# Performance work log

Measured on AMD Instinct MI355X. Metric: run time of the kernel, lower is better.

Reference implementation:

```python
import jax, jax.numpy as jnp
import numpy as np

HEADS = 8
DIM_HEAD = 64
LA = 0.33
LD = 0.33
LG = 0.33


def setup_inputs() -> dict:
    key = jax.random.key(0)
    ks = jax.random.split(key, 6)
    B, N, D = 4, 1024, 512
    inner = HEADS * DIM_HEAD
    x = jax.random.normal(ks[0], (B, N, D), jnp.float32)
    mask = jax.random.uniform(ks[1], (B, N)) < 0.9
    # sparse 0/1 molecular adjacency
    adjacency_mat = (jax.random.uniform(ks[2], (B, N, N)) < 0.05).astype(jnp.float32)
    # positive pairwise distances
    distance_mat = jax.random.uniform(ks[3], (B, N, N), jnp.float32) * 5.0
    W_qkv = jax.random.normal(ks[4], (D, inner * 3), jnp.float32) * 0.02
    W_out = jax.random.normal(ks[5], (inner, D), jnp.float32) * 0.02
    b_out = jnp.zeros((D,), jnp.float32)
    return {"x": x, "mask": mask, "adjacency_mat": adjacency_mat,
            "distance_mat": distance_mat, "W_qkv": W_qkv, "W_out": W_out, "b_out": b_out}


def reference(x, mask, adjacency_mat, distance_mat, W_qkv, W_out, b_out):
    B, N, _ = x.shape
    scale = DIM_HEAD ** -0.5
    # 'b n (h qkv d)' split: reshape to (B, N, H, 3, Dh) then move heads forward
    qkv = (x @ W_qkv).reshape(B, N, HEADS, 3, DIM_HEAD)
    q, k, v = (jnp.transpose(qkv[..., i, :], (0, 2, 1, 3)) for i in range(3))
    dots = jnp.einsum('bhid,bhjd->bhij', q, k) * scale  # [B,H,N,N]
    big = jnp.finfo(dots.dtype).max
    m2 = mask[:, None, :, None] & mask[:, None, None, :]  # [B,1,N,N]
    dots = jnp.where(m2, dots, -big)
    attn = jax.nn.softmax(dots, axis=-1) * LA
    # adjacency masked to 0; distance masked to +max so exp(-t) -> 0
    adj = jnp.where(m2, adjacency_mat[:, None], 0.0)
    dist = jnp.where(m2, distance_mat[:, None], big)
    attn = attn + LG * adj + LD * jnp.exp(-dist)
    out = jnp.einsum('bhij,bhjd->bhid', attn, v)
    out = jnp.transpose(out, (0, 2, 1, 3)).reshape(B, N, HEADS * DIM_HEAD)
    return out @ W_out + b_out
```

## Files before the change

### kernel.cpp

```cpp
#include <hip/hip_runtime.h>
#include <hip/hip_bf16.h>

typedef __attribute__((ext_vector_type(8))) __bf16 bf16x8;
typedef __attribute__((ext_vector_type(8))) unsigned short ushort8;
typedef __attribute__((ext_vector_type(4))) float f32x4;

#define DEVFN static __device__ __forceinline__

constexpr int B_ = 4, N_ = 1024, H_ = 8, DH_ = 64, INNER_ = 512, QC_ = 1536;
constexpr float LA_ = 0.33f, LD_ = 0.33f, LG_ = 0.33f;
constexpr float SCALE2_ = 0.125f * 1.44269504088896f;
constexpr long OCP_STRIDE_ = (long)4096 * 512;
constexpr long LP_STRIDE_  = (long)4 * 8 * 1024;

DEVFN unsigned short f2b(float f){
  unsigned int u = __builtin_bit_cast(unsigned int, f);
  u += 0x7FFFu + ((u >> 16) & 1u);
  return (unsigned short)(u >> 16);
}
DEVFN float b2f(unsigned short s){
  unsigned int u = ((unsigned int)s) << 16;
  return __builtin_bit_cast(float, u);
}
DEVFN float fexp2(float x){
  float r; asm("v_exp_f32 %0, %1" : "=v"(r) : "v"(x)); return r;
}
DEVFN unsigned int pack2(float lo, float hi){
  union { unsigned int u; __bf16 h[2]; } z;
  z.h[0] = (__bf16)lo; z.h[1] = (__bf16)hi;
  return z.u;
}

DEVFN f32x4 mfma16(bf16x8 a, bf16x8 b, f32x4 c){
  return __builtin_amdgcn_mfma_f32_16x16x32_bf16(a, b, c, 0, 0, 0);
}

DEVFN bf16x8 ldsb8(const unsigned short* p){ return *(const bf16x8*)p; }

DEVFN void gload16(const unsigned short* g, unsigned short* l){
  __builtin_amdgcn_global_load_lds(
      (const __attribute__((address_space(1))) unsigned int*)g,
      (__attribute__((address_space(3))) unsigned int*)l, 16, 0, 0);
}


DEVFN int detect_enc_w0(const unsigned char* m8, const int* m32, const float* mf,
                        int t, int* fsh){
  if (t < 64){
    unsigned char a = m8[t];
    int bb = m32[t];
    float c = mf[t];
    unsigned long long bad0 = __ballot(a > 1);
    unsigned long long one0 = __ballot(a == 1);
    unsigned long long bad1 = __ballot(bb != 0 && bb != 1);
    unsigned long long one1 = __ballot(bb == 1);
    unsigned long long bad2 = __ballot(c != 0.0f && c != 1.0f);
    unsigned long long one2 = __ballot(c == 1.0f);
    if (t == 0){
      int f = 0;
      if (bad0 == 0ull && __popcll(one0) > 42) f = 0;
      else if (bad1 == 0ull && __popcll(one1) > 42) f = 1;
      else if (bad2 == 0ull && __popcll(one2) > 42) f = 2;
      *fsh = f;
    }
  }
  __syncthreads();
  return *fsh;
}

__global__ void prep_k(const unsigned char* __restrict__ m8, const int* __restrict__ m32,
                       const float* __restrict__ mf, unsigned char* __restrict__ mv,
                       const float* __restrict__ x, unsigned short* __restrict__ xb,
                       const float* __restrict__ Wq, unsigned short* __restrict__ WqT,
                       const float* __restrict__ Wo, unsigned short* __restrict__ WoT,
                       const float* __restrict__ adj, const float* __restrict__ dist,
                       unsigned short* __restrict__ Madd)
{
  const int bid = blockIdx.x, t = threadIdx.x;
  if (bid < 16){
    __shared__ int fsh;
    int f = detect_enc_w0(m8, m32, mf, t, &fsh);
    int i = bid * 256 + t;
    unsigned char v;
    if (f == 0) v = (m8[i] != 0);
    else if (f == 1) v = (m32[i] != 0);
    else v = (mf[i] != 0.0f);
    mv[i] = v;
  } else if (bid < 2064){
    int i = (bid - 16) * 256 + t;
    float4 v = ((const float4*)x)[i];
    ushort4 o = { f2b(v.x), f2b(v.y), f2b(v.z), f2b(v.w) };
    ((ushort4*)xb)[i] = o;
  } else if (bid < 3088){
    const float* W; unsigned short* Wt; int K, Nn, bx, by;
    if (bid < 2832){ W = Wq; Wt = WqT; K = 512; Nn = 1536; int r = bid - 2064; bx = r % 48; by = r / 48; }
    else           { W = Wo; Wt = WoT; K = 512; Nn = 512;  int r = bid - 2832; bx = r % 16; by = r / 16; }
    __shared__ float tt[32][33];
    int nb = bx * 32, kb = by * 32;
    int tx = t & 31, ty = t >> 5;
    #pragma unroll
    for (int i = 0; i < 32; i += 8)
      tt[ty + i][tx] = W[(long)(kb + ty + i) * Nn + nb + tx];
    __syncthreads();
    #pragma unroll
    for (int i = 0; i < 32; i += 8)
      Wt[(long)(nb + ty + i) * K + kb + tx] = f2b(tt[tx][ty + i]);
  } else {
    __shared__ int fsh;
    int f = detect_enc_w0(m8, m32, mf, t, &fsh);

    long i = (long)(bid - 3088) * 256 + t;
    long e = i * 4;
    int b = (int)(e >> 20);
    int rem = (int)(e & (long)(N_ * N_ - 1));
    int row = rem >> 10, col0 = rem & (N_ - 1);
    float4 a = ((const float4*)adj)[i];
    float4 d = ((const float4*)dist)[i];
    bool mi, mc[4];
    if (f == 0){
      mi = m8[b * N_ + row] != 0;
      unsigned int pk = *(const unsigned int*)(m8 + b * N_ + col0);
      #pragma unroll
      for (int r = 0; r < 4; r++) mc[r] = ((pk >> (8 * r)) & 255u) != 0;
    } else if (f == 1){
      mi = m32[b * N_ + row] != 0;
      #pragma unroll
      for (int r = 0; r < 4; r++) mc[r] = m32[b * N_ + col0 + r] != 0;
    } else {
      mi = mf[b * N_ + row] != 0.0f;
      #pragma unroll
      for (int r = 0; r < 4; r++) mc[r] = mf[b * N_ + col0 + r] != 0.0f;
    }
    float va[4] = {a.x, a.y, a.z, a.w};
    float vd[4] = {d.x, d.y, d.z, d.w};
    ushort4 o;
    unsigned short* op = (unsigned short*)&o;
    #pragma unroll
    for (int r = 0; r < 4; r++){
      bool m2 = mi && mc[r];
      float v = m2 ? (LG_ * va[r] + LD_ * __expf(-vd[r])) : 0.0f;
      op[r] = f2b(v);
    }
    ((ushort4*)Madd)[i] = o;
  }
}

template<int MODE, int BM, int BN>
__global__ __launch_bounds__(256)
void gemm_bt_k(const unsigned short* __restrict__ A, const unsigned short* __restrict__ Bt,
               const float* __restrict__ Cin, void* __restrict__ Cout,
               const unsigned short* __restrict__ Op, const float* __restrict__ Lp,
               unsigned short* __restrict__ VtOut,
               int M, int Nn, int K, long azs, long bzs)
{
  constexpr int BK = 64;
  constexpr int WM = BM / 2, WN = BN / 2, MR = WM / 16, NR = WN / 16;
  __shared__ __attribute__((aligned(16))) unsigned short As[2][BM * BK];
  __shared__ __attribute__((aligned(16))) unsigned short Bs[2][BN * BK];
  const int bm = blockIdx.x * BM, bn = blockIdx.y * BN, z = blockIdx.z;
  const unsigned short* Ap = A + (long)z * azs;
  const unsigned short* Bp = Bt + (long)z * bzs;
  const int tid = threadIdx.x, w = tid >> 6, lane = tid & 63;
  const int l15 = lane & 15, lg = lane >> 4;
  const int wr = w >> 1, wc = w & 1;
  const int srow = lane >> 3;
  const int sk0 = ((lane & 7) ^ srow) * 8;
  const int rk0 = (lg ^ (l15 & 7)) * 8;
  const int rk1 = ((lg + 4) ^ (l15 & 7)) * 8;

  f32x4 acc[MR][NR] = {};

  for (int kk = 0;;){
    if (kk == 0){
      #pragma unroll
      for (int i = 0; i < BM / 32; i++){
        int r0 = i * 32 + w * 8;
        gload16(Ap + (long)(bm + r0 + srow) * K + sk0, &As[0][r0 * BK]);
      }
      #pragma unroll
      for (int i = 0; i < BN / 32; i++){
        int r0 = i * 32 + w * 8;
        gload16(Bp + (long)(bn + r0 + srow) * K + sk0, &Bs[0][r0 * BK]);
      }
      __syncthreads();
    }
    int cur = (kk / BK) & 1;
    if (kk + BK < K){
      #pragma unroll
      for (int i = 0; i < BM / 32; i++){
        int r0 = i * 32 + w * 8;
        gload16(Ap + (long)(bm + r0 + srow) * K + (kk + BK) + sk0, &As[cur ^ 1][r0 * BK]);
      }
      #pragma unroll
      for (int i = 0; i < BN / 32; i++){
        int r0 = i * 32 + w * 8;
        gload16(Bp + (long)(bn + r0 + srow) * K + (kk + BK) + sk0, &Bs[cur ^ 1][r0 * BK]);
      }
    }
    bf16x8 af[MR][2], bf[NR][2];
    #pragma unroll
    for (int m = 0; m < MR; m++){
      const unsigned short* p = &As[cur][(wr * WM + m * 16 + l15) * BK];
      af[m][0] = ldsb8(p + rk0); af[m][1] = ldsb8(p + rk1);
    }
    #pragma unroll
    for (int n = 0; n < NR; n++){
      const unsigned short* p = &Bs[cur][(wc * WN + n * 16 + l15) * BK];
      bf[n][0] = ldsb8(p + rk0); bf[n][1] = ldsb8(p + rk1);
    }
    #pragma unroll
    for (int m = 0; m < MR; m++)
      #pragma unroll
      for (int n = 0; n < NR; n++){
        acc[m][n] = mfma16(af[m][0], bf[n][0], acc[m][n]);
        acc[m][n] = mfma16(af[m][1], bf[n][1], acc[m][n]);
      }
    kk += BK;
    if (kk >= K) break;
    __syncthreads();
  }

  #pragma unroll
  for (int m = 0; m < MR; m++)
    #pragma unroll
    for (int n = 0; n < NR; n++){
      int row0 = bm + wr * WM + m * 16 + lg * 4;
      int col = bn + wc * WN + n * 16 + l15;
      if (MODE == 0){
        ushort4 o;
        unsigned short* op = (unsigned short*)&o;
        #pragma unroll
        for (int r = 0; r < 4; r++){
          op[r] = f2b(acc[m][n][r]);
          ((unsigned short*)Cout)[(long)(row0 + r) * Nn + col] = op[r];
        }
        int hm = col % 192;
        if (hm >= 128){
          int bb = row0 >> 10, j0 = row0 & (N_ - 1);
          int hd = (col / 192) * 64 + (hm - 128);
          *(ushort4*)(VtOut + ((long)bb * INNER_ + hd) * N_ + j0) = o;
        }
      } else if (MODE == 1){
        #pragma unroll
        for (int r = 0; r < 4; r++){
          int row = row0 + r;
          float v = acc[m][n][r];
          long obase = ((long)z * N_ + row) * INNER_ + col;
          float o = b2f(Op[obase]) + b2f(Op[OCP_STRIDE_ + obase]);
          long lbase = ((long)z * H_ + (col >> 6)) * N_ + row;
          float l = Lp[lbase] + Lp[LP_STRIDE_ + lbase];
          v += LA_ * o / l;
          ((unsigned short*)Cout)[((long)z * N_ + row) * Nn + col] = f2b(v);
        }
      } else {
        #pragma unroll
        for (int r = 0; r < 4; r++)
          ((float*)Cout)[(long)(row0 + r) * Nn + col] = acc[m][n][r] + Cin[col];
      }
    }
}

__global__ __launch_bounds__(256)
void attn2_k(const unsigned short* __restrict__ QKV, const unsigned short* __restrict__ Vt,
             const unsigned char* __restrict__ mv,
             unsigned short* __restrict__ Ocp, float* __restrict__ Lp)
{
  __shared__ __attribute__((aligned(16))) unsigned short Ks[64][72];
  __shared__ __attribute__((aligned(16))) unsigned short Vs[64][72];
  __shared__ __attribute__((aligned(16))) unsigned short Ps[4][16][72];
  const int qb = blockIdx.x * 64, h = blockIdx.y;
  const int b = blockIdx.z & 3, js = blockIdx.z >> 2;
  const int tid = threadIdx.x, w = tid >> 6, lane = tid & 63;
  const int l15 = lane & 15, lg = lane >> 4;
  const int rs = l15 & 7;

  const long qrowA = (long)(b * N_ + qb + w * 16 + l15) * QC_ + h * 192;
  bf16x8 qf0 = *(const bf16x8*)(QKV + qrowA + lg * 8);
  bf16x8 qf1 = *(const bf16x8*)(QKV + qrowA + 32 + lg * 8);

  const bool rv1 = mv[b * N_ + qb + w * 16 + l15] != 0;

  float l_run = 0.f;
  f32x4 acc[4] = {};

  const unsigned short* Vbase = Vt + ((long)b * INNER_ + h * DH_) * N_;
  const int kr0 = tid >> 3, kr1 = kr0 + 32;
  const int kb = tid & 7;
  const int ko = kb * 8;
  const int ws = ((kb ^ (kr0 & 7)) * 8);

  ushort8 kreg0, kreg1, vreg0, vreg1;
  {
    const int jb0 = js * 512;
    kreg0 = *(const ushort8*)(QKV + (long)(b * N_ + jb0 + kr0) * QC_ + h * 192 + 64 + ko);
    kreg1 = *(const ushort8*)(QKV + (long)(b * N_ + jb0 + kr1) * QC_ + h * 192 + 64 + ko);
    vreg0 = *(const ushort8*)(Vbase + (long)kr0 * N_ + jb0 + ko);
    vreg1 = *(const ushort8*)(Vbase + (long)kr1 * N_ + jb0 + ko);
  }

  for (int jt = 0; jt < 8; jt++){
    const int jbase = js * 512 + jt * 64;
    __syncthreads();
    *(ushort8*)&Ks[kr0][ws] = kreg0;
    *(ushort8*)&Ks[kr1][ws] = kreg1;
    *(ushort8*)&Vs[kr0][ws] = vreg0;
    *(ushort8*)&Vs[kr1][ws] = vreg1;
    if (jt < 7){
      const int jn = jbase + 64;
      kreg0 = *(const ushort8*)(QKV + (long)(b * N_ + jn + kr0) * QC_ + h * 192 + 64 + ko);
      kreg1 = *(const ushort8*)(QKV + (long)(b * N_ + jn + kr1) * QC_ + h * 192 + 64 + ko);
      vreg0 = *(const ushort8*)(Vbase + (long)kr0 * N_ + jn + ko);
      vreg1 = *(const ushort8*)(Vbase + (long)kr1 * N_ + jn + ko);
    }
    __syncthreads();

    f32x4 s[4];
    __builtin_amdgcn_s_setprio(1);
    #pragma unroll
    for (int ct = 0; ct < 4; ct++){
      bf16x8 k0 = ldsb8(&Ks[ct * 16 + l15][(lg ^ rs) * 8]);
      bf16x8 k1 = ldsb8(&Ks[ct * 16 + l15][((4 + lg) ^ rs) * 8]);
      f32x4 zz = {};
      zz = mfma16(k0, qf0, zz);
      zz = mfma16(k1, qf1, zz);
      s[ct] = zz;
    }
    __builtin_amdgcn_s_setprio(0);

    unsigned int cvm[4];
    #pragma unroll
    for (int ct = 0; ct < 4; ct++)
      cvm[ct] = *(const unsigned int*)(mv + b * N_ + jbase + ct * 16 + lg * 4);

    float tsum = 0.f;
    unsigned int pw[4][2];
    #pragma unroll
    for (int ct = 0; ct < 4; ct++){
      float pv[4];
      #pragma unroll
      for (int r = 0; r < 4; r++){
        float x = s[ct][r] * SCALE2_;
        bool ck = ((cvm[ct] >> (8 * r)) & 255u) != 0;
        float sv = ck ? x : -3e38f;
        if (!rv1) sv = 0.0f;
        float p = fexp2(sv);
        tsum += p;
        pv[r] = p;
      }
      pw[ct][0] = pack2(pv[0], pv[1]);
      pw[ct][1] = pack2(pv[2], pv[3]);
    }
    tsum += __shfl_xor(tsum, 16);
    tsum += __shfl_xor(tsum, 32);
    l_run += tsum;

    #pragma unroll
    for (int ct = 0; ct < 4; ct++)
      #pragma unroll
      for (int p2 = 0; p2 < 2; p2++){
        int klo = ct * 16 + lg * 4 + 2 * p2;
        int kp = ((klo >> 3) ^ rs) * 8 + (klo & 7);
        *(unsigned int*)&Ps[w][l15][kp] = pw[ct][p2];
      }

    asm volatile("s_waitcnt lgkmcnt(0)" ::: "memory");
    __builtin_amdgcn_sched_barrier(0);

    bf16x8 pf0 = ldsb8(&Ps[w][l15][(lg ^ rs) * 8]);
    bf16x8 pf1 = ldsb8(&Ps[w][l15][((4 + lg) ^ rs) * 8]);
    __builtin_amdgcn_s_setprio(1);
    #pragma unroll
    for (int ct = 0; ct < 4; ct++){
      bf16x8 v0 = ldsb8(&Vs[ct * 16 + l15][(lg ^ rs) * 8]);
      bf16x8 v1 = ldsb8(&Vs[ct * 16 + l15][((4 + lg) ^ rs) * 8]);
      acc[ct] = mfma16(pf0, v0, acc[ct]);
      acc[ct] = mfma16(pf1, v1, acc[ct]);
    }
    __builtin_amdgcn_s_setprio(0);
  }

  #pragma unroll
  for (int r = 0; r < 4; r++){
    long orow = (long)js * OCP_STRIDE_ / INNER_ + b * N_ + qb + w * 16 + lg * 4 + r;
    #pragma unroll
    for (int ct = 0; ct < 4; ct++)
      Ocp[orow * INNER_ + h * DH_ + ct * 16 + l15] = f2b(acc[ct][r]);
  }
  if (lg == 0)
    Lp[(long)js * LP_STRIDE_ + ((long)b * H_ + h) * N_ + qb + w * 16 + l15] = l_run;
}

extern "C" void kernel_launch(void* const* d_in, const int* in_sizes, int n_in,
                              void* d_out, int out_size, void* d_ws, size_t ws_size,
                              hipStream_t stream)
{
  const float* x    = (const float*)d_in[0];
  const void*  msk  = d_in[1];
  const float* adj  = (const float*)d_in[2];
  const float* dst  = (const float*)d_in[3];
  const float* wqkv = (const float*)d_in[4];
  const float* wout = (const float*)d_in[5];
  const float* bout = (const float*)d_in[6];
  float* out = (float*)d_out;

  char* p = (char*)d_ws;
  unsigned short* QKV  = (unsigned short*)p;  p += (long)4096 * 1536 * 2;
  unsigned short* Xb   = (unsigned short*)p;  p += (long)4096 * 512 * 2;
  unsigned short* WqT  = (unsigned short*)p;  p += (long)1536 * 512 * 2;
  unsigned short* WoT  = (unsigned short*)p;  p += (long)512 * 512 * 2;
  unsigned short* Vt   = (unsigned short*)p;  p += (long)4 * 512 * 1024 * 2;
  unsigned short* Madd = (unsigned short*)p;  p += (long)4 * 1024 * 1024 * 2;
  unsigned short* Ocp  = (unsigned short*)p;  p += (long)2 * OCP_STRIDE_ * 2;
  float*          Lp   = (float*)p;           p += (long)2 * LP_STRIDE_ * 4;
  unsigned short* OcB  = (unsigned short*)p;  p += (long)4096 * 512 * 2;
  unsigned char*  mv   = (unsigned char*)p;   p += 4096;

  prep_k<<<7184, 256, 0, stream>>>((const unsigned char*)msk, (const int*)msk,
                                   (const float*)msk, mv, x, Xb, wqkv, WqT, wout, WoT,
                                   adj, dst, Madd);
  gemm_bt_k<0, 128, 64><<<dim3(32, 24, 1), 256, 0, stream>>>(
      Xb, WqT, nullptr, QKV, nullptr, nullptr, Vt, 4096, 1536, 512, 0, 0);
  attn2_k<<<dim3(16, 8, 8), 256, 0, stream>>>(QKV, Vt, mv, Ocp, Lp);
  gemm_bt_k<1, 64, 64><<<dim3(16, 8, 4), 256, 0, stream>>>(
      Madd, Vt, nullptr, OcB, Ocp, Lp, nullptr, 1024, 512, 1024,
      (long)1024 * 1024, (long)512 * 1024);
  gemm_bt_k<2, 64, 64><<<dim3(64, 8, 1), 256, 0, stream>>>(
      OcB, WoT, bout, out, nullptr, nullptr, nullptr, 4096, 512, 512, 0, 0);
}
```

Before: 80.06 us.

## Move Madd precompute from prep kernel into attention kernel grid

The adjacency/distance mask-add (Madd) computation moves out of the prep kernel and runs as extra blocks appended to the attention kernel's flattened 1D grid. The bandwidth-bound Madd blocks can then overlap with the compute-bound attention blocks instead of sitting on the serial path before the QKV GEMM. The attention block index decoding changes from a 3D grid to a flattened index. The detect scratch reuses the Ps shared buffer. A risk is that attention blocks now share the GPU with memory-heavy blocks, which may interfere with them.

```diff
diff --git a/kernel.cpp b/kernel.cpp
--- a/kernel.cpp
+++ b/kernel.cpp
@@ -72,9 +72,7 @@
                        const float* __restrict__ mf, unsigned char* __restrict__ mv,
                        const float* __restrict__ x, unsigned short* __restrict__ xb,
                        const float* __restrict__ Wq, unsigned short* __restrict__ WqT,
-                       const float* __restrict__ Wo, unsigned short* __restrict__ WoT,
-                       const float* __restrict__ adj, const float* __restrict__ dist,
-                       unsigned short* __restrict__ Madd)
+                       const float* __restrict__ Wo, unsigned short* __restrict__ WoT)
 {
   const int bid = blockIdx.x, t = threadIdx.x;
   if (bid < 16){
@@ -91,7 +89,7 @@
     float4 v = ((const float4*)x)[i];
     ushort4 o = { f2b(v.x), f2b(v.y), f2b(v.z), f2b(v.w) };
     ((ushort4*)xb)[i] = o;
-  } else if (bid < 3088){
+  } else {
     const float* W; unsigned short* Wt; int K, Nn, bx, by;
     if (bid < 2832){ W = Wq; Wt = WqT; K = 512; Nn = 1536; int r = bid - 2064; bx = r % 48; by = r / 48; }
     else           { W = Wo; Wt = WoT; K = 512; Nn = 512;  int r = bid - 2832; bx = r % 16; by = r / 16; }
@@ -105,43 +103,6 @@
     #pragma unroll
     for (int i = 0; i < 32; i += 8)
       Wt[(long)(nb + ty + i) * K + kb + tx] = f2b(tt[tx][ty + i]);
-  } else {
-    __shared__ int fsh;
-    int f = detect_enc_w0(m8, m32, mf, t, &fsh);
-
-    long i = (long)(bid - 3088) * 256 + t;
-    long e = i * 4;
-    int b = (int)(e >> 20);
-    int rem = (int)(e & (long)(N_ * N_ - 1));
-    int row = rem >> 10, col0 = rem & (N_ - 1);
-    float4 a = ((const float4*)adj)[i];
-    float4 d = ((const float4*)dist)[i];
-    bool mi, mc[4];
-    if (f == 0){
-      mi = m8[b * N_ + row] != 0;
-      unsigned int pk = *(const unsigned int*)(m8 + b * N_ + col0);
-      #pragma unroll
-      for (int r = 0; r < 4; r++) mc[r] = ((pk >> (8 * r)) & 255u) != 0;
-    } else if (f == 1){
-      mi = m32[b * N_ + row] != 0;
-      #pragma unroll
-      for (int r = 0; r < 4; r++) mc[r] = m32[b * N_ + col0 + r] != 0;
-    } else {
-      mi = mf[b * N_ + row] != 0.0f;
-      #pragma unroll
-      for (int r = 0; r < 4; r++) mc[r] = mf[b * N_ + col0 + r] != 0.0f;
-    }
-    float va[4] = {a.x, a.y, a.z, a.w};
-    float vd[4] = {d.x, d.y, d.z, d.w};
-    ushort4 o;
-    unsigned short* op = (unsigned short*)&o;
-    #pragma unroll
-    for (int r = 0; r < 4; r++){
-      bool m2 = mi && mc[r];
-      float v = m2 ? (LG_ * va[r] + LD_ * __expf(-vd[r])) : 0.0f;
-      op[r] = f2b(v);
-    }
-    ((ushort4*)Madd)[i] = o;
   }
 }
 
@@ -261,16 +222,61 @@
 }
 
 __global__ __launch_bounds__(256)
-void attn2_k(const unsigned short* __restrict__ QKV, const unsigned short* __restrict__ Vt,
-             const unsigned char* __restrict__ mv,
-             unsigned short* __restrict__ Ocp, float* __restrict__ Lp)
+void attn_madd_k(const unsigned short* __restrict__ QKV, const unsigned short* __restrict__ Vt,
+                 const unsigned char* __restrict__ mv,
+                 unsigned short* __restrict__ Ocp, float* __restrict__ Lp,
+                 const unsigned char* __restrict__ m8, const int* __restrict__ m32,
+                 const float* __restrict__ mf,
+                 const float* __restrict__ adj, const float* __restrict__ dist,
+                 unsigned short* __restrict__ Madd)
 {
   __shared__ __attribute__((aligned(16))) unsigned short Ks[64][72];
   __shared__ __attribute__((aligned(16))) unsigned short Vs[64][72];
   __shared__ __attribute__((aligned(16))) unsigned short Ps[4][16][72];
-  const int qb = blockIdx.x * 64, h = blockIdx.y;
-  const int b = blockIdx.z & 3, js = blockIdx.z >> 2;
-  const int tid = threadIdx.x, w = tid >> 6, lane = tid & 63;
+  const int bid = blockIdx.x, tid = threadIdx.x;
+
+  if (bid >= 1024){
+    int f = detect_enc_w0(m8, m32, mf, tid, (int*)&Ps[0][0][0]);
+    long i = (long)(bid - 1024) * 256 + tid;
+    long e = i * 4;
+    int b = (int)(e >> 20);
+    int rem = (int)(e & (long)(N_ * N_ - 1));
+    int row = rem >> 10, col0 = rem & (N_ - 1);
+    float4 a = ((const float4*)adj)[i];
+    float4 d = ((const float4*)dist)[i];
+    bool mi, mc[4];
+    if (f == 0){
+      mi = m8[b * N_ + row] != 0;
+      unsigned int pk = *(const unsigned int*)(m8 + b * N_ + col0);
+      #pragma unroll
+      for (int r = 0; r < 4; r++) mc[r] = ((pk >> (8 * r)) & 255u) != 0;
+    } else if (f == 1){
+      mi = m32[b * N_ + row] != 0;
+      #pragma unroll
+      for (int r = 0; r < 4; r++) mc[r] = m32[b * N_ + col0 + r] != 0;
+    } else {
+      mi = mf[b * N_ + row] != 0.0f;
+      #pragma unroll
+      for (int r = 0; r < 4; r++) mc[r] = mf[b * N_ + col0 + r] != 0.0f;
+    }
+    float va[4] = {a.x, a.y, a.z, a.w};
+    float vd[4] = {d.x, d.y, d.z, d.w};
+    ushort4 o;
+    unsigned short* op = (unsigned short*)&o;
+    #pragma unroll
+    for (int r = 0; r < 4; r++){
+      bool m2 = mi && mc[r];
+      float v = m2 ? (LG_ * va[r] + LD_ * __expf(-vd[r])) : 0.0f;
+      op[r] = f2b(v);
+    }
+    ((ushort4*)Madd)[i] = o;
+    return;
+  }
+
+  const int qb = (bid & 15) * 64, h = (bid >> 4) & 7;
+  const int zc = bid >> 7;
+  const int b = zc & 3, js = zc >> 2;
+  const int w = tid >> 6, lane = tid & 63;
   const int l15 = lane & 15, lg = lane >> 4;
   const int rs = l15 & 7;
 
@@ -415,12 +421,13 @@
   unsigned short* OcB  = (unsigned short*)p;  p += (long)4096 * 512 * 2;
   unsigned char*  mv   = (unsigned char*)p;   p += 4096;
 
-  prep_k<<<7184, 256, 0, stream>>>((const unsigned char*)msk, (const int*)msk,
-                                   (const float*)msk, mv, x, Xb, wqkv, WqT, wout, WoT,
-                                   adj, dst, Madd);
+  prep_k<<<3088, 256, 0, stream>>>((const unsigned char*)msk, (const int*)msk,
+                                   (const float*)msk, mv, x, Xb, wqkv, WqT, wout, WoT);
   gemm_bt_k<0, 128, 64><<<dim3(32, 24, 1), 256, 0, stream>>>(
       Xb, WqT, nullptr, QKV, nullptr, nullptr, Vt, 4096, 1536, 512, 0, 0);
-  attn2_k<<<dim3(16, 8, 8), 256, 0, stream>>>(QKV, Vt, mv, Ocp, Lp);
+  attn_madd_k<<<5120, 256, 0, stream>>>(QKV, Vt, mv, Ocp, Lp,
+                                        (const unsigned char*)msk, (const int*)msk,
+                                        (const float*)msk, adj, dst, Madd);
   gemm_bt_k<1, 64, 64><<<dim3(16, 8, 4), 256, 0, stream>>>(
       Madd, Vt, nullptr, OcB, Ocp, Lp, nullptr, 1024, 512, 1024,
       (long)1024 * 1024, (long)512 * 1024);
```

After: 78.16 us. 2.4% less time.
